# Kernel tuning notes

Measured on AMD Instinct MI355X. Metric: run time of the kernel, lower is better.

## Reference

```python
import jax, jax.numpy as jnp
import numpy as np

N, C, T, V, E = 4, 64, 64, 1024, 4096
IN_CH, OUT_CH, H = 256, 512, 8
DH = OUT_CH // H


def _leaky(x):
    return jnp.where(x >= 0, x, 0.01 * x)


def _mlp(x, w1, b1, w2, b2, g, b):
    # Linear -> LeakyReLU -> (dropout: eval identity) -> Linear -> BatchNorm(batch stats) -> LeakyReLU
    h = _leaky(x @ w1 + b1)
    h = h @ w2 + b2
    n, e, f = h.shape
    flat = h.reshape(n * e, f)
    mu = flat.mean(0)
    var = flat.var(0)  # biased variance, as torch BatchNorm uses for normalization
    flat = (flat - mu) * jax.lax.rsqrt(var + 1e-5) * g + b
    return _leaky(flat.reshape(n, e, f))


def _attn(q, k, v, wq, bq, wk, bk, wv, bv, wf, bf):
    # SelfAttention with scale=1: embed dim == OUT_CH, H heads of DH dims
    n, lq, _ = q.shape
    def split(t):
        return t.reshape(n, -1, H, DH).transpose(0, 2, 1, 3)  # (n, H, L, DH)
    Q = split(q @ wq + bq)
    K = split(k @ wk + bk)
    Vv = split(v @ wv + bv)
    scale = jnp.sqrt(jnp.float32(DH))
    att = jax.nn.softmax(jnp.einsum("nhqd,nhkd->nhqk", Q, K) / scale, axis=-1)
    x = jnp.einsum("nhqk,nhkd->nhqd", att, Vv)
    x = x.transpose(0, 2, 1, 3).reshape(n, lq, OUT_CH)
    return x @ wf + bf


def setup_inputs():
    key = jax.random.key(0)
    ks = list(jax.random.split(key, 24))

    def lin(k1, n_in, n_out):
        w = jax.random.normal(k1, (n_in, n_out), jnp.float32) * np.sqrt(2.0 / (n_in + n_out))
        b = jnp.full((n_out,), 0.1, jnp.float32)
        return w, b

    inp = {
        "x1": jax.random.normal(ks[0], (N, C, T, V), jnp.float32),
        "x2": jax.random.normal(ks[1], (N, C, T, V), jnp.float32),
        "encode1": jax.random.uniform(ks[2], (E, V), dtype=jnp.float32),
        "encode2": jax.random.uniform(ks[3], (E, V), dtype=jnp.float32),
    }
    i = 4
    for name in ("mlp", "nlp"):
        inp[name + "_w1"], inp[name + "_b1"] = lin(ks[i], 2 * IN_CH, OUT_CH); i += 1
        inp[name + "_w2"], inp[name + "_b2"] = lin(ks[i], OUT_CH, OUT_CH); i += 1
        inp[name + "_gamma"] = jnp.ones((OUT_CH,), jnp.float32)
        inp[name + "_beta"] = jnp.zeros((OUT_CH,), jnp.float32)
    for name in ("att1", "att2"):
        for p in ("wq", "wk", "wv", "fc"):
            inp[name + "_" + p + "_w"], inp[name + "_" + p + "_b"] = lin(ks[i], OUT_CH, OUT_CH); i += 1
    return inp


def reference(x1, x2, encode1, encode2,
              mlp_w1, mlp_b1, mlp_w2, mlp_b2, mlp_gamma, mlp_beta,
              nlp_w1, nlp_b1, nlp_w2, nlp_b2, nlp_gamma, nlp_beta,
              att1_wq_w, att1_wq_b, att1_wk_w, att1_wk_b, att1_wv_w, att1_wv_b, att1_fc_w, att1_fc_b,
              att2_wq_w, att2_wq_b, att2_wk_w, att2_wk_b, att2_wv_w, att2_wv_b, att2_fc_w, att2_fc_b):
    n, c, t, v = x1.shape

    def prep(x):
        # permute(0,2,3,1).view(N,V,-1) then AdaptiveAvgPool1d(IN_CH) with exact windows
        x = jnp.transpose(x, (0, 2, 3, 1)).reshape(n, v, t * c)
        return x.reshape(n, v, IN_CH, (t * c) // IN_CH).mean(-1)

    x1p = prep(x1)
    x2p = prep(x2)

    def node_enc(x):
        return jnp.concatenate([
            jnp.einsum("ev,nvc->nec", encode1, x),
            jnp.einsum("ev,nvc->nec", encode2, x),
        ], axis=-1)  # (N, E, 2*IN_CH)

    h1 = _mlp(node_enc(x1p), mlp_w1, mlp_b1, mlp_w2, mlp_b2, mlp_gamma, mlp_beta)
    h2 = _mlp(node_enc(x2p), nlp_w1, nlp_b1, nlp_w2, nlp_b2, nlp_gamma, nlp_beta)

    def edge_enc(h):
        r = jnp.einsum("ev,nec->nvc", encode1, h)  # (N, V, OUT_CH)
        return r / r.shape[1]

    e1 = edge_enc(h1)
    e2 = edge_enc(h2)

    a1 = _attn(e2, e1, e1, att1_wq_w, att1_wq_b, att1_wk_w, att1_wk_b, att1_wv_w, att1_wv_b, att1_fc_w, att1_fc_b)
    a2 = _attn(e1, e2, e2, att2_wq_w, att2_wq_b, att2_wk_w, att2_wk_b, att2_wv_w, att2_wv_b, att2_fc_w, att2_fc_b)

    c1 = jnp.concatenate([a1, a2], axis=1)  # (N, 2V, OUT_CH)
    c2 = jnp.concatenate([a2, a1], axis=1)
    A = jax.nn.softmax(jnp.einsum("nic,njc->nij", c1, c2), axis=-1)  # (N, 2V, 2V)
    # normalize_dynamic_digraph: AGCN-style column-degree normalization A @ D^{-1}
    col = A.sum(axis=1, keepdims=True)
    return A * jnp.where(col > 0, 1.0 / col, 0.0)
```

## Files before the change

kernel.cpp:

```cpp
#include <hip/hip_runtime.h>
#include <hip/hip_bf16.h>

#define LEAKY(v) ((v) >= 0.f ? (v) : 0.01f * (v))

typedef __attribute__((ext_vector_type(8))) short short8b;
typedef __attribute__((ext_vector_type(4))) float f32x4;
typedef __attribute__((ext_vector_type(4))) unsigned short us4;

__device__ __forceinline__ unsigned short f2b(float f) {
  unsigned int u = __builtin_bit_cast(unsigned int, f);
  return (unsigned short)((u + 0x7FFFu + ((u >> 16) & 1u)) >> 16);
}
__device__ __forceinline__ float b2f(unsigned short s) {
  return __builtin_bit_cast(float, (unsigned int)s << 16);
}

__device__ __forceinline__ void gload16(const unsigned short* g, unsigned short* l) {
  __builtin_amdgcn_global_load_lds(
      (const __attribute__((address_space(1))) unsigned int*)(g),
      (__attribute__((address_space(3))) unsigned int*)(l), 16, 0, 0);
}

__device__ __forceinline__ void stage64(const unsigned short* g, int ldg,
                                        unsigned short* lds, int lane, int w) {
  const int r8 = lane >> 3;
  const int ce = ((lane & 7) ^ r8) << 3;
  const int r0 = w * 8 + r8;
  gload16(g + (long)r0 * ldg + ce, lds + w * 512);
  gload16(g + (long)(r0 + 32) * ldg + ce, lds + 2048 + w * 512);
}

__device__ __forceinline__ short8b ldsw(const unsigned short* base, int row, int c4) {
  return *(const short8b*)&base[row * 64 + (((c4 ^ (row & 7)) << 3))];
}

struct WPtrs { const float* p[12]; float sc[12]; };

__global__ __launch_bounds__(256) void prologue_misc(
    const float* __restrict__ X1, const float* __restrict__ X2,
    float* __restrict__ S, const float* __restrict__ enc1,
    const float* __restrict__ enc2, unsigned short* __restrict__ ENC,
    unsigned short* __restrict__ E1T, WPtrs wp,
    unsigned short* __restrict__ WT) {
  __shared__ float t[64][65];
  const int b = blockIdx.x;
  const int tid = threadIdx.x;
  if (b < 2048) {
#pragma unroll
    for (int it = 0; it < 4; ++it) {
      const int lb = b + it * 2048;
      const int tt = lb & 63, y = (lb >> 6) & 15, z = lb >> 10;
      const float* X = (z >> 2) ? X2 : X1;
      const int n = z & 3;
      const long base = (((long)n * 64 + y * 4) * 64 + tt) * 1024 + tid * 4;
      const float4 a = *(const float4*)&X[base];
      const float4 bb = *(const float4*)&X[base + 65536];
      const float4 c = *(const float4*)&X[base + 2 * 65536];
      const float4 d = *(const float4*)&X[base + 3 * 65536];
      float4 o;
      o.x = (a.x + bb.x) + (c.x + d.x);
      o.y = (a.y + bb.y) + (c.y + d.y);
      o.z = (a.z + bb.z) + (c.z + d.z);
      o.w = (a.w + bb.w) + (c.w + d.w);
      *(float4*)&S[(((long)z * 16 + y) * 64 + tt) * 1024 + tid * 4] = o;
    }
  } else if (b < 4096) {
#pragma unroll
    for (int it = 0; it < 4; ++it) {
      const int cb = (b - 2048) + it * 2048;
      const int z = cb >> 12;
      const float* in = z ? enc2 : enc1;
      unsigned short* o = ENC + (long)z * (4L << 20);
      const long i = (long)(cb & 4095) * 256 + tid;
      const float4 v = ((const float4*)in)[i];
      us4 q;
      q[0] = f2b(v.x); q[1] = f2b(v.y); q[2] = f2b(v.z); q[3] = f2b(v.w);
      ((us4*)o)[i] = q;
    }
  } else if (b < 5120) {
    const int b3 = b - 4096;
    const int c0 = (b3 & 15) * 64, r0 = (b3 >> 4) * 64;
#pragma unroll
    for (int it = 0; it < 4; ++it) {
      int idx = tid + it * 256;
      int r = idx >> 4, c4 = (idx & 15) * 4;
      float4 v = *(const float4*)&enc1[(long)(r0 + r) * 1024 + c0 + c4];
      t[c4 + 0][r] = v.x; t[c4 + 1][r] = v.y;
      t[c4 + 2][r] = v.z; t[c4 + 3][r] = v.w;
    }
    __syncthreads();
#pragma unroll
    for (int it = 0; it < 4; ++it) {
      int idx = tid + it * 256;
      int c = idx >> 4, r4 = (idx & 15) * 4;
      us4 o;
      o[0] = f2b(t[c][r4 + 0]); o[1] = f2b(t[c][r4 + 1]);
      o[2] = f2b(t[c][r4 + 2]); o[3] = f2b(t[c][r4 + 3]);
      *(us4*)&E1T[(long)(c0 + c) * 4096 + r0 + r4] = o;
    }
  } else {
    const int b4 = b - 5120;
    const int x = b4 & 7, y = (b4 >> 3) & 7, z = b4 >> 6;
    const float* in = wp.p[z];
    const float s = wp.sc[z];
    unsigned short* ob = WT + (long)z * 262144;
    const int c0 = x * 64, r0 = y * 64;
#pragma unroll
    for (int it = 0; it < 4; ++it) {
      int idx = tid + it * 256;
      int r = idx >> 4, c4 = (idx & 15) * 4;
      float4 v = *(const float4*)&in[(long)(r0 + r) * 512 + c0 + c4];
      t[c4 + 0][r] = v.x; t[c4 + 1][r] = v.y;
      t[c4 + 2][r] = v.z; t[c4 + 3][r] = v.w;
    }
    __syncthreads();
#pragma unroll
    for (int it = 0; it < 4; ++it) {
      int idx = tid + it * 256;
      int c = idx >> 4, r4 = (idx & 15) * 4;
      us4 o;
      o[0] = f2b(t[c][r4 + 0] * s); o[1] = f2b(t[c][r4 + 1] * s);
      o[2] = f2b(t[c][r4 + 2] * s); o[3] = f2b(t[c][r4 + 3] * s);
      *(us4*)&ob[(long)(c0 + c) * 512 + r0 + r4] = o;
    }
  }
}

__global__ __launch_bounds__(256) void prep_finish(const float* __restrict__ S,
                                                   unsigned short* __restrict__ Pt) {
  const int t = blockIdx.x;
  const int cbi = blockIdx.y;
  const int z = blockIdx.z;
  const int n = z & 3, inp = z >> 2;
  const int tid = threadIdx.x;
  __shared__ unsigned short sacc[64][20];
  const long sb = (((long)z * 16 + cbi * 4) * 64 + t) * 1024 + tid * 4;
  const float4 a = *(const float4*)&S[sb];
  const float4 b = *(const float4*)&S[sb + 65536];
  const float4 c = *(const float4*)&S[sb + 2 * 65536];
  const float4 d = *(const float4*)&S[sb + 3 * 65536];
  float acc[4];
  acc[0] = (a.x + b.x) + (c.x + d.x);
  acc[1] = (a.y + b.y) + (c.y + d.y);
  acc[2] = (a.z + b.z) + (c.z + d.z);
  acc[3] = (a.w + b.w) + (c.w + d.w);
  const int q = tid & 15, vb = tid >> 4;
#pragma unroll
  for (int j = 0; j < 4; ++j)
    sacc[q * 4 + j][vb] = f2b(acc[j] * (1.f / 16.f));
  __syncthreads();
  const int vvv = tid >> 2, iq = tid & 3;
  const us4 o = *(const us4*)&sacc[vvv][iq * 4];
  *(us4*)&Pt[(long)inp * (1L << 20) + (long)n * 262144 +
             (long)(vvv * 4 + cbi) * 1024 + t * 16 + iq * 4] = o;
}

__global__ __launch_bounds__(256) void addcvt4(const unsigned short* __restrict__ P,
                                               unsigned short* __restrict__ out) {
#pragma unroll
  for (int it = 0; it < 4; ++it) {
    const long i = ((long)(blockIdx.x + it * 1024) * 256 + threadIdx.x) * 4;
    const us4 a = *(const us4*)&P[i];
    const us4 b = *(const us4*)&P[i + 4194304];
    const us4 c = *(const us4*)&P[i + 2 * 4194304];
    const us4 d = *(const us4*)&P[i + 3 * 4194304];
    us4 o;
#pragma unroll
    for (int j = 0; j < 4; ++j)
      o[j] = f2b((b2f(a[j]) + b2f(b[j])) + (b2f(c[j]) + b2f(d[j])));
    *(us4*)&out[i] = o;
  }
}

struct GDesc { const unsigned short* A; const unsigned short* B; long coff;
               const float* bias; int mode; float bscale; };
struct GDescs { GDesc d[16]; };

template <int ACT, int CMODE, int KSPLIT>
__global__ __launch_bounds__(256) void gemm_z(
    GDescs ga, void* __restrict__ Cv, int K, int lda, int ldb, int ldc,
    long sC2, float alpha) {
  const int bz = blockIdx.z;
  const int s = (KSPLIT > 1) ? (bz % KSPLIT) : 0;
  const int zb = (KSPLIT > 1) ? (bz / KSPLIT) : bz;
  const GDesc g = ga.d[zb];
  const unsigned short* Ab = g.A + (long)s * K;
  const unsigned short* Bb = g.B + (long)s * K;
  const int m0 = blockIdx.y * 128, n0 = blockIdx.x * 128;
  const int tid = threadIdx.x;
  const int lane = tid & 63, w = tid >> 6;
  const int wr = (w >> 1) * 64, wc = (w & 1) * 64;
  __shared__ unsigned short As[128 * 64];
  __shared__ unsigned short Bs[128 * 64];
  f32x4 acc[4][4];
#pragma unroll
  for (int i = 0; i < 4; ++i)
#pragma unroll
    for (int j = 0; j < 4; ++j) acc[i][j] = (f32x4){0.f, 0.f, 0.f, 0.f};
  const int srow = tid >> 3;
  const int scol = (((tid & 7) ^ ((tid >> 3) & 7)) << 3);
  const int rl = lane & 15, lg = lane >> 4, rx = rl & 7;
  for (int k0 = 0; k0 < K; k0 += 64) {
    __syncthreads();
#pragma unroll
    for (int it = 0; it < 4; ++it) {
      gload16(Ab + (long)(m0 + it * 32 + srow) * lda + k0 + scol,
              As + w * 512 + it * 2048);
      gload16(Bb + (long)(n0 + it * 32 + srow) * ldb + k0 + scol,
              Bs + w * 512 + it * 2048);
    }
    __syncthreads();
#pragma unroll
    for (int kk = 0; kk < 2; ++kk) {
      short8b af[4], bfr[4];
#pragma unroll
      for (int m = 0; m < 4; ++m)
        af[m] = *(const short8b*)&As[(wr + m * 16 + rl) * 64 +
                                     ((((kk * 4 + lg) ^ rx)) << 3)];
#pragma unroll
      for (int nn = 0; nn < 4; ++nn)
        bfr[nn] = *(const short8b*)&Bs[(wc + nn * 16 + rl) * 64 +
                                       ((((kk * 4 + lg) ^ rx)) << 3)];
#pragma unroll
      for (int m = 0; m < 4; ++m)
#pragma unroll
        for (int nn = 0; nn < 4; ++nn)
          acc[m][nn] = __builtin_amdgcn_mfma_f32_16x16x32_bf16(
              af[m], bfr[nn], acc[m][nn], 0, 0, 0);
    }
  }
  const int rrow = lg * 4;
  float bv[4];
#pragma unroll
  for (int nn = 0; nn < 4; ++nn)
    bv[nn] = g.bias ? g.bias[n0 + wc + nn * 16 + rl] * g.bscale : 0.f;
  const bool vt_layout = (CMODE == 2) || (CMODE == 4 && g.mode == 2);
  if (CMODE == 2 || CMODE == 4) {
    if (vt_layout) {
#pragma unroll
      for (int m = 0; m < 4; ++m)
#pragma unroll
        for (int nn = 0; nn < 4; ++nn) {
          const int row = m0 + wr + m * 16 + rrow;
          const int col = n0 + wc + nn * 16 + rl;
          us4 o;
#pragma unroll
          for (int r = 0; r < 4; ++r) {
            float v = alpha * acc[m][nn][r] + bv[nn];
            if (ACT == 1) v = LEAKY(v);
            o[r] = f2b(v);
          }
          const long off = g.coff + (long)(row >> 10) * 524288 +
                           (long)col * 1024 + (row & 1023);
          *(us4*)&((unsigned short*)Cv)[off] = o;
        }
    } else {
#pragma unroll
      for (int m = 0; m < 4; ++m)
#pragma unroll
        for (int nn = 0; nn < 4; ++nn)
#pragma unroll
          for (int r = 0; r < 4; ++r) {
            float v = alpha * acc[m][nn][r] + bv[nn];
            if (ACT == 1) v = LEAKY(v);
            const long off = g.coff +
                             (long)(m0 + wr + m * 16 + rrow + r) * ldc + n0 +
                             wc + nn * 16 + rl;
            ((unsigned short*)Cv)[off] = f2b(v);
          }
    }
  } else if (CMODE == 3) {
#pragma unroll
    for (int m = 0; m < 4; ++m)
#pragma unroll
      for (int nn = 0; nn < 4; ++nn) {
        const int row = m0 + wr + m * 16 + rrow;
        const int col = n0 + wc + nn * 16 + rl;
        us4 o;
#pragma unroll
        for (int r = 0; r < 4; ++r) {
          float v = alpha * acc[m][nn][r] + bv[nn];
          if (ACT == 1) v = LEAKY(v);
          o[r] = f2b(v);
        }
        *(us4*)&((unsigned short*)Cv)[g.coff + (long)col * ldc + row] = o;
      }
  } else {
#pragma unroll
    for (int m = 0; m < 4; ++m)
#pragma unroll
      for (int nn = 0; nn < 4; ++nn)
#pragma unroll
        for (int r = 0; r < 4; ++r) {
          float v = alpha * acc[m][nn][r] + bv[nn];
          if (ACT == 1) v = LEAKY(v);
          long off = g.coff + (long)s * sC2 +
                     (long)(m0 + wr + m * 16 + rrow + r) * ldc + n0 + wc +
                     nn * 16 + rl;
          if (CMODE == 1)
            ((unsigned short*)Cv)[off] = f2b(v);
          else
            ((float*)Cv)[off] = v;
        }
  }
}

__global__ __launch_bounds__(256) void bn_fused(
    unsigned short* __restrict__ X,
    const float* __restrict__ g1, const float* __restrict__ be1,
    const float* __restrict__ g2, const float* __restrict__ be2) {
  const int f = blockIdx.x;
  const int z = blockIdx.z;
  unsigned short* p = X + (long)z * (8L << 20) + (long)f * 16384;
  const int tid = threadIdx.x;
  us4 v[16];
  float s = 0.f, q = 0.f;
#pragma unroll
  for (int k = 0; k < 16; ++k) {
    v[k] = *(const us4*)&p[(k * 256 + tid) * 4];
#pragma unroll
    for (int j = 0; j < 4; ++j) {
      const float x = b2f(v[k][j]);
      s += x; q += x * x;
    }
  }
#pragma unroll
  for (int mask = 1; mask < 64; mask <<= 1) {
    s += __shfl_xor(s, mask, 64);
    q += __shfl_xor(q, mask, 64);
  }
  __shared__ float rs[8];
  const int wv = tid >> 6;
  if ((tid & 63) == 0) { rs[wv] = s; rs[4 + wv] = q; }
  __syncthreads();
  s = rs[0] + rs[1] + rs[2] + rs[3];
  q = rs[4] + rs[5] + rs[6] + rs[7];
  const float mu = s * (1.f / 16384.f);
  const float var = q * (1.f / 16384.f) - mu * mu;
  const float gg = (z ? g2 : g1)[f];
  const float bb0 = (z ? be2 : be1)[f];
  const float rstd = rsqrtf(var + 1e-5f) * gg;
  const float bb = bb0 - mu * rstd;
#pragma unroll
  for (int k = 0; k < 16; ++k) {
    us4 o;
#pragma unroll
    for (int j = 0; j < 4; ++j) {
      const float y = b2f(v[k][j]) * rstd + bb;
      o[j] = f2b(LEAKY(y));
    }
    *(us4*)&p[(k * 256 + tid) * 4] = o;
  }
}

__global__ __launch_bounds__(256) void attn_mfma(
    const unsigned short* __restrict__ Q, const unsigned short* __restrict__ K,
    const unsigned short* __restrict__ Vt, unsigned short* __restrict__ O) {
  const int qb = blockIdx.x, h = blockIdx.y;
  const int n = blockIdx.z & 3, sel = blockIdx.z >> 2;
  Q += (long)sel * 4194304;
  K += (long)sel * 4194304;
  Vt += (long)sel * 2097152;
  O += (long)sel * 2097152;
  const int tid = threadIdx.x;
  const int lane = tid & 63, w = tid >> 6;
  const int rl = lane & 15, lg = lane >> 4;
  __shared__ unsigned short Qs[4096];
  __shared__ unsigned short Ks[4096];
  __shared__ unsigned short Vs[4096];
  __shared__ unsigned short Ps[4096];
  stage64(Q + ((long)n * 1024 + qb * 64) * 512 + h * 64, 512, Qs, lane, w);
  __syncthreads();
  const int q = w * 16 + rl;
  const short8b qr0 = ldsw(Qs, q, lg);
  const short8b qr1 = ldsw(Qs, q, 4 + lg);
  float l_r = 0.f;
  f32x4 po[4];
#pragma unroll
  for (int i = 0; i < 4; ++i) po[i] = (f32x4){0.f, 0.f, 0.f, 0.f};
  const unsigned short* Kg0 = K + ((long)n * 1024) * 512 + h * 64;
  const unsigned short* Vg0 = Vt + (long)n * 524288 + (long)(h * 64) * 1024;
  for (int kt = 0; kt < 16; ++kt) {
    __syncthreads();
    stage64(Kg0 + (long)(kt * 64) * 512, 512, Ks, lane, w);
    stage64(Vg0 + kt * 64, 1024, Vs, lane, w);
    __syncthreads();
    f32x4 sa[4];
#pragma unroll
    for (int i = 0; i < 4; ++i) sa[i] = (f32x4){0.f, 0.f, 0.f, 0.f};
#pragma unroll
    for (int kk = 0; kk < 2; ++kk) {
      const short8b qf = kk ? qr1 : qr0;
#pragma unroll
      for (int mt = 0; mt < 4; ++mt) {
        const short8b kf = ldsw(Ks, mt * 16 + rl, 4 * kk + lg);
        sa[mt] = __builtin_amdgcn_mfma_f32_16x16x32_bf16(kf, qf, sa[mt], 0, 0, 0);
      }
    }
    float ps = 0.f;
#pragma unroll
    for (int mt = 0; mt < 4; ++mt) {
      us4 o;
#pragma unroll
      for (int r = 0; r < 4; ++r) {
        const float p = exp2f(sa[mt][r]);
        ps += p;
        o[r] = f2b(p);
      }
      const int c16 = (4 * mt + lg) >> 1;
      *(us4*)&Ps[q * 64 + ((c16 ^ (q & 7)) << 3) + ((lg & 1) << 2)] = o;
    }
    ps += __shfl_xor(ps, 16, 64);
    ps += __shfl_xor(ps, 32, 64);
    l_r += ps;
#pragma unroll
    for (int kk = 0; kk < 2; ++kk) {
      const short8b pf = ldsw(Ps, q, 4 * kk + lg);
#pragma unroll
      for (int nt = 0; nt < 4; ++nt) {
        const short8b vf = ldsw(Vs, nt * 16 + rl, 4 * kk + lg);
        po[nt] = __builtin_amdgcn_mfma_f32_16x16x32_bf16(pf, vf, po[nt], 0, 0, 0);
      }
    }
  }
  float invr[4];
#pragma unroll
  for (int r = 0; r < 4; ++r) invr[r] = 1.f / __shfl(l_r, lg * 4 + r, 64);
  const long ob = ((long)n * 1024 + qb * 64 + w * 16) * 512 + h * 64;
#pragma unroll
  for (int nt = 0; nt < 4; ++nt)
#pragma unroll
    for (int r = 0; r < 4; ++r)
      O[ob + (long)(lg * 4 + r) * 512 + nt * 16 + rl] = f2b(po[nt][r] * invr[r]);
}

__global__ __launch_bounds__(256) void softmax_cs(const float* __restrict__ D,
                                                  float* __restrict__ RS,
                                                  float* __restrict__ CS) {
  __shared__ float colacc[2048];
  __shared__ float red[8];
  const int tid = threadIdx.x;
  const int wv = tid >> 6, ln = tid & 63;
#pragma unroll
  for (int k = 0; k < 8; ++k) colacc[tid + k * 256] = 0.f;
  __syncthreads();
  const int r0 = blockIdx.x * 8;
  const int n = r0 >> 11;
  for (int rr = 0; rr < 8; ++rr) {
    const float* p = D + (long)(r0 + rr) * 2048;
    float v[8];
    float mx = -1e30f;
#pragma unroll
    for (int k = 0; k < 8; ++k) {
      v[k] = p[tid + k * 256];
      mx = fmaxf(mx, v[k]);
    }
#pragma unroll
    for (int mask = 1; mask < 64; mask <<= 1) mx = fmaxf(mx, __shfl_xor(mx, mask, 64));
    if (ln == 0) red[wv] = mx;
    __syncthreads();
    mx = fmaxf(fmaxf(red[0], red[1]), fmaxf(red[2], red[3]));
    float sum = 0.f;
#pragma unroll
    for (int k = 0; k < 8; ++k) {
      v[k] = __expf(v[k] - mx);
      sum += v[k];
    }
#pragma unroll
    for (int mask = 1; mask < 64; mask <<= 1) sum += __shfl_xor(sum, mask, 64);
    if (ln == 0) red[4 + wv] = sum;
    __syncthreads();
    sum = red[4] + red[5] + red[6] + red[7];
    const float inv = 1.f / sum;
    if (tid == 0) {
      RS[(r0 + rr) * 2] = mx;
      RS[(r0 + rr) * 2 + 1] = inv;
    }
#pragma unroll
    for (int k = 0; k < 8; ++k) colacc[tid + k * 256] += v[k] * inv;
    __syncthreads();
  }
#pragma unroll
  for (int k = 0; k < 8; ++k)
    atomicAdd(&CS[n * 2048 + tid + k * 256], colacc[tid + k * 256]);
}

__global__ __launch_bounds__(256) void final_scale(float* __restrict__ D,
                                                   const float* __restrict__ RS,
                                                   const float* __restrict__ CS) {
#pragma unroll
  for (int it = 0; it < 8; ++it) {
    const long i = ((long)(blockIdx.x + it * 2048) * 256 + threadIdx.x) * 4;
    const long row = i >> 11;
    const int n = (int)(row >> 11);
    const int j = (int)(i & 2047);
    const float mx = RS[row * 2];
    const float inv = RS[row * 2 + 1];
    float4 v = *(float4*)&D[i];
    const float* c = &CS[n * 2048 + j];
    v.x = __expf(v.x - mx) * inv * (c[0] > 0.f ? 1.f / c[0] : 0.f);
    v.y = __expf(v.y - mx) * inv * (c[1] > 0.f ? 1.f / c[1] : 0.f);
    v.z = __expf(v.z - mx) * inv * (c[2] > 0.f ? 1.f / c[2] : 0.f);
    v.w = __expf(v.w - mx) * inv * (c[3] > 0.f ? 1.f / c[3] : 0.f);
    *(float4*)&D[i] = v;
  }
}

extern "C" void kernel_launch(void* const* d_in, const int* in_sizes, int n_in,
                              void* d_out, int out_size, void* d_ws,
                              size_t ws_size, hipStream_t stream) {
  const float* x1 = (const float*)d_in[0];
  const float* x2 = (const float*)d_in[1];
  const float* enc1 = (const float*)d_in[2];
  const float* enc2 = (const float*)d_in[3];
  const float* mlp_b1 = (const float*)d_in[5];
  const float* mlp_b2 = (const float*)d_in[7];
  const float* mlp_g = (const float*)d_in[8];
  const float* mlp_be = (const float*)d_in[9];
  const float* nlp_b1 = (const float*)d_in[11];
  const float* nlp_b2 = (const float*)d_in[13];
  const float* nlp_g = (const float*)d_in[14];
  const float* nlp_be = (const float*)d_in[15];
  float* out = (float*)d_out;

  unsigned short* W = (unsigned short*)d_ws;
  const long M1 = 1L << 20;
  const long S = 262144;
  const float K2 = 0.18033688f;
  unsigned short* Pt = W;
  unsigned short* ENC = W + 4 * M1;
  unsigned short* E1T = W + 12 * M1;
  unsigned short* WT = W + 16 * M1;
  unsigned short* NE = W + 20 * M1;
  unsigned short* H1T = W + 20 * M1;
  unsigned short* MID = W + 36 * M1;
  float* Sprep = (float*)(W + 36 * M1);
  unsigned short* PB = W + 36 * M1;
  unsigned short* E1 = W + 4 * M1;
  unsigned short* E2 = W + 6 * M1;
  unsigned short* QKV = W + 36 * M1;
  unsigned short* VT = W + 44 * M1;
  unsigned short* AO = W + 48 * M1;
  unsigned short* A1P = W + 8 * M1;
  unsigned short* A2P = W + 10 * M1;
  float* ST = (float*)(W + 56 * M1);
  float* CS = ST + 2048;
  float* RS = CS + 8192;

  const dim3 T(256);
  const long sP = 262144;
  const long sNE = 2097152;
  const long sE = 524288;
  const long sD = 4194304;

  hipMemsetAsync(CS, 0, 8192 * sizeof(float), stream);

  WPtrs wp;
  wp.p[0] = (const float*)d_in[4];   wp.sc[0] = 1.f;
  wp.p[1] = (const float*)d_in[6];   wp.sc[1] = 1.f;
  wp.p[2] = (const float*)d_in[10];  wp.sc[2] = 1.f;
  wp.p[3] = (const float*)d_in[12];  wp.sc[3] = 1.f;
  wp.p[4] = (const float*)d_in[16];  wp.sc[4] = K2;
  wp.p[5] = (const float*)d_in[18];  wp.sc[5] = 1.f;
  wp.p[6] = (const float*)d_in[24];  wp.sc[6] = K2;
  wp.p[7] = (const float*)d_in[26];  wp.sc[7] = 1.f;
  wp.p[8] = (const float*)d_in[20];  wp.sc[8] = 1.f;
  wp.p[9] = (const float*)d_in[28];  wp.sc[9] = 1.f;
  wp.p[10] = (const float*)d_in[22]; wp.sc[10] = 1.f;
  wp.p[11] = (const float*)d_in[30]; wp.sc[11] = 1.f;
  prologue_misc<<<5888, T, 0, stream>>>(x1, x2, Sprep, enc1, enc2, ENC, E1T,
                                        wp, WT);
  prep_finish<<<dim3(64, 4, 8), T, 0, stream>>>(Sprep, Pt);

  {
    GDescs g{};
    for (int inp = 0; inp < 2; ++inp)
      for (int pr = 0; pr < 2; ++pr)
        for (int nn = 0; nn < 4; ++nn)
          g.d[inp * 8 + pr * 4 + nn] = {
              ENC + (long)pr * (4 * M1), Pt + (long)inp * M1 + nn * sP,
              (long)inp * (8 * M1) + (long)nn * sNE + pr * 256, nullptr, 0, 1.f};
    gemm_z<0, 1, 1><<<dim3(2, 32, 16), T, 0, stream>>>(g, NE, 1024, 1024,
                                                       1024, 512, 0, 1.f);
  }
  {
    GDescs g{};
    g.d[0] = {NE, WT + 0 * S, 0, mlp_b1, 0, 1.f};
    g.d[1] = {NE + 8 * M1, WT + 2 * S, 8 * M1, nlp_b1, 0, 1.f};
    gemm_z<1, 1, 1><<<dim3(4, 128, 2), T, 0, stream>>>(g, MID, 512, 512, 512,
                                                       512, 0, 1.f);
  }
  {
    GDescs g{};
    g.d[0] = {MID, WT + 1 * S, 0, mlp_b2, 0, 1.f};
    g.d[1] = {MID + 8 * M1, WT + 3 * S, 8 * M1, nlp_b2, 0, 1.f};
    gemm_z<0, 3, 1><<<dim3(4, 128, 2), T, 0, stream>>>(g, H1T, 512, 512, 512,
                                                       16384, 0, 1.f);
  }
  bn_fused<<<dim3(512, 1, 2), T, 0, stream>>>(H1T, mlp_g, mlp_be, nlp_g, nlp_be);

  {
    GDescs g{};
    for (int d = 0; d < 8; ++d)
      g.d[d] = {E1T, H1T + (long)(d >> 2) * (8 * M1) + (d & 3) * 4096,
                (long)d * 524288, nullptr, 0, 1.f};
    gemm_z<0, 1, 4><<<dim3(4, 8, 32), T, 0, stream>>>(g, PB, 1024, 4096,
                                                      16384, 512, 4194304,
                                                      1.f / 1024.f);
  }
  addcvt4<<<1024, T, 0, stream>>>(PB, E1);

  {
    GDescs g{};
    g.d[0] = {E2, WT + 4 * S, 0, (const float*)d_in[17], 1, K2};
    g.d[1] = {E1, WT + 5 * S, 2 * M1, (const float*)d_in[19], 1, 1.f};
    g.d[2] = {E1, WT + 6 * S, 4 * M1, (const float*)d_in[25], 1, K2};
    g.d[3] = {E2, WT + 7 * S, 6 * M1, (const float*)d_in[27], 1, 1.f};
    g.d[4] = {E1, WT + 8 * S, 8 * M1, (const float*)d_in[21], 2, 1.f};
    g.d[5] = {E2, WT + 9 * S, 10 * M1, (const float*)d_in[29], 2, 1.f};
    gemm_z<0, 4, 1><<<dim3(4, 32, 6), T, 0, stream>>>(g, QKV, 512, 512, 512,
                                                      512, 0, 1.f);
  }

  attn_mfma<<<dim3(16, 8, 8), T, 0, stream>>>(QKV, QKV + 2 * M1, VT, AO);

  {
    GDescs g{};
    g.d[0] = {AO, WT + 10 * S, 0, (const float*)d_in[23], 0, 1.f};
    g.d[1] = {AO + 2 * M1, WT + 11 * S, 2 * M1, (const float*)d_in[31], 0, 1.f};
    gemm_z<0, 1, 1><<<dim3(4, 32, 2), T, 0, stream>>>(g, A1P, 512, 512, 512,
                                                      512, 0, 1.f);
  }

  {
    GDescs g{};
    for (int q = 0; q < 4; ++q)
      for (int n = 0; n < 4; ++n) {
        const unsigned short* A = (q < 2 ? A1P : A2P) + n * sE;
        const unsigned short* B = ((q == 0 || q == 2) ? A2P : A1P) + n * sE;
        const long coff =
            (long)n * sD + (q & 1) * 1024 + (long)(q >> 1) * 2097152;
        g.d[q * 4 + n] = {A, B, coff, nullptr, 0, 1.f};
      }
    gemm_z<0, 0, 1><<<dim3(8, 8, 16), T, 0, stream>>>(g, out, 512, 512, 512,
                                                      2048, 0, 1.f);
  }

  softmax_cs<<<1024, T, 0, stream>>>(out, RS, CS);
  final_scale<<<2048, T, 0, stream>>>(out, RS, CS);
}
```

Before: 382.9 us.

## Pool input in one pass and split the fused prologue into separate kernels

The channel pooling of x1/x2 used to be two stages: a partial sum written to a float scratch buffer, then read back by a finish kernel. Each block now loads all 16 channel slices directly and reduces them in registers, so the intermediate scratch write and re-read disappear. The fused multi-role prologue kernel is also split into separate kernels for pooling, encoder bf16 conversion, encoder transpose and weight transpose, with occupancy hints on some of them. The cost is more kernel launches and higher register pressure in the pooling kernel, which holds 16 float4 loads per thread.

```diff
diff --git a/kernel.cpp b/kernel.cpp
--- a/kernel.cpp
+++ b/kernel.cpp
@@ -34,125 +34,111 @@
   return *(const short8b*)&base[row * 64 + (((c4 ^ (row & 7)) << 3))];
 }
 
-struct WPtrs { const float* p[12]; float sc[12]; };
-
-__global__ __launch_bounds__(256) void prologue_misc(
+__global__ __launch_bounds__(256, 4) void prep_pool_t(
     const float* __restrict__ X1, const float* __restrict__ X2,
-    float* __restrict__ S, const float* __restrict__ enc1,
-    const float* __restrict__ enc2, unsigned short* __restrict__ ENC,
-    unsigned short* __restrict__ E1T, WPtrs wp,
-    unsigned short* __restrict__ WT) {
-  __shared__ float t[64][65];
-  const int b = blockIdx.x;
-  const int tid = threadIdx.x;
-  if (b < 2048) {
-#pragma unroll
-    for (int it = 0; it < 4; ++it) {
-      const int lb = b + it * 2048;
-      const int tt = lb & 63, y = (lb >> 6) & 15, z = lb >> 10;
-      const float* X = (z >> 2) ? X2 : X1;
-      const int n = z & 3;
-      const long base = (((long)n * 64 + y * 4) * 64 + tt) * 1024 + tid * 4;
-      const float4 a = *(const float4*)&X[base];
-      const float4 bb = *(const float4*)&X[base + 65536];
-      const float4 c = *(const float4*)&X[base + 2 * 65536];
-      const float4 d = *(const float4*)&X[base + 3 * 65536];
-      float4 o;
-      o.x = (a.x + bb.x) + (c.x + d.x);
-      o.y = (a.y + bb.y) + (c.y + d.y);
-      o.z = (a.z + bb.z) + (c.z + d.z);
-      o.w = (a.w + bb.w) + (c.w + d.w);
-      *(float4*)&S[(((long)z * 16 + y) * 64 + tt) * 1024 + tid * 4] = o;
-    }
-  } else if (b < 4096) {
-#pragma unroll
-    for (int it = 0; it < 4; ++it) {
-      const int cb = (b - 2048) + it * 2048;
-      const int z = cb >> 12;
-      const float* in = z ? enc2 : enc1;
-      unsigned short* o = ENC + (long)z * (4L << 20);
-      const long i = (long)(cb & 4095) * 256 + tid;
-      const float4 v = ((const float4*)in)[i];
-      us4 q;
-      q[0] = f2b(v.x); q[1] = f2b(v.y); q[2] = f2b(v.z); q[3] = f2b(v.w);
-      ((us4*)o)[i] = q;
-    }
-  } else if (b < 5120) {
-    const int b3 = b - 4096;
-    const int c0 = (b3 & 15) * 64, r0 = (b3 >> 4) * 64;
-#pragma unroll
-    for (int it = 0; it < 4; ++it) {
-      int idx = tid + it * 256;
-      int r = idx >> 4, c4 = (idx & 15) * 4;
-      float4 v = *(const float4*)&enc1[(long)(r0 + r) * 1024 + c0 + c4];
-      t[c4 + 0][r] = v.x; t[c4 + 1][r] = v.y;
-      t[c4 + 2][r] = v.z; t[c4 + 3][r] = v.w;
-    }
-    __syncthreads();
-#pragma unroll
-    for (int it = 0; it < 4; ++it) {
-      int idx = tid + it * 256;
-      int c = idx >> 4, r4 = (idx & 15) * 4;
-      us4 o;
-      o[0] = f2b(t[c][r4 + 0]); o[1] = f2b(t[c][r4 + 1]);
-      o[2] = f2b(t[c][r4 + 2]); o[3] = f2b(t[c][r4 + 3]);
-      *(us4*)&E1T[(long)(c0 + c) * 4096 + r0 + r4] = o;
-    }
-  } else {
-    const int b4 = b - 5120;
-    const int x = b4 & 7, y = (b4 >> 3) & 7, z = b4 >> 6;
-    const float* in = wp.p[z];
-    const float s = wp.sc[z];
-    unsigned short* ob = WT + (long)z * 262144;
-    const int c0 = x * 64, r0 = y * 64;
-#pragma unroll
-    for (int it = 0; it < 4; ++it) {
-      int idx = tid + it * 256;
-      int r = idx >> 4, c4 = (idx & 15) * 4;
-      float4 v = *(const float4*)&in[(long)(r0 + r) * 512 + c0 + c4];
-      t[c4 + 0][r] = v.x; t[c4 + 1][r] = v.y;
-      t[c4 + 2][r] = v.z; t[c4 + 3][r] = v.w;
-    }
-    __syncthreads();
-#pragma unroll
-    for (int it = 0; it < 4; ++it) {
-      int idx = tid + it * 256;
-      int c = idx >> 4, r4 = (idx & 15) * 4;
-      us4 o;
-      o[0] = f2b(t[c][r4 + 0] * s); o[1] = f2b(t[c][r4 + 1] * s);
-      o[2] = f2b(t[c][r4 + 2] * s); o[3] = f2b(t[c][r4 + 3] * s);
-      *(us4*)&ob[(long)(c0 + c) * 512 + r0 + r4] = o;
-    }
-  }
-}
-
-__global__ __launch_bounds__(256) void prep_finish(const float* __restrict__ S,
-                                                   unsigned short* __restrict__ Pt) {
+    unsigned short* __restrict__ Pt) {
   const int t = blockIdx.x;
   const int cbi = blockIdx.y;
-  const int z = blockIdx.z;
-  const int n = z & 3, inp = z >> 2;
+  const int n = blockIdx.z & 3, inp = blockIdx.z >> 2;
+  const float* X = inp ? X2 : X1;
   const int tid = threadIdx.x;
   __shared__ unsigned short sacc[64][20];
-  const long sb = (((long)z * 16 + cbi * 4) * 64 + t) * 1024 + tid * 4;
-  const float4 a = *(const float4*)&S[sb];
-  const float4 b = *(const float4*)&S[sb + 65536];
-  const float4 c = *(const float4*)&S[sb + 2 * 65536];
-  const float4 d = *(const float4*)&S[sb + 3 * 65536];
-  float acc[4];
-  acc[0] = (a.x + b.x) + (c.x + d.x);
-  acc[1] = (a.y + b.y) + (c.y + d.y);
-  acc[2] = (a.z + b.z) + (c.z + d.z);
-  acc[3] = (a.w + b.w) + (c.w + d.w);
+  const long base0 = (((long)n * 64 + cbi * 16) * 64 + t) * 1024 + tid * 4;
+  f32x4 v[16];
+#pragma unroll
+  for (int m = 0; m < 16; ++m)
+    v[m] = *(const f32x4*)&X[base0 + (long)m * 65536];
   const int q = tid & 15, vb = tid >> 4;
 #pragma unroll
-  for (int j = 0; j < 4; ++j)
-    sacc[q * 4 + j][vb] = f2b(acc[j] * (1.f / 16.f));
+  for (int j = 0; j < 4; ++j) {
+    float s = ((v[0][j] + v[1][j]) + (v[2][j] + v[3][j])) +
+              ((v[4][j] + v[5][j]) + (v[6][j] + v[7][j]));
+    s += ((v[8][j] + v[9][j]) + (v[10][j] + v[11][j])) +
+         ((v[12][j] + v[13][j]) + (v[14][j] + v[15][j]));
+    sacc[q * 4 + j][vb] = f2b(s * (1.f / 16.f));
+  }
   __syncthreads();
   const int vvv = tid >> 2, iq = tid & 3;
   const us4 o = *(const us4*)&sacc[vvv][iq * 4];
   *(us4*)&Pt[(long)inp * (1L << 20) + (long)n * 262144 +
              (long)(vvv * 4 + cbi) * 1024 + t * 16 + iq * 4] = o;
+}
+
+__global__ __launch_bounds__(256, 4) void convert2_f2b(
+    const float* __restrict__ i1, const float* __restrict__ i2,
+    unsigned short* __restrict__ out) {
+  const int tid = threadIdx.x;
+  f32x4 v[4];
+  long oidx[4];
+#pragma unroll
+  for (int it = 0; it < 4; ++it) {
+    const int cb = blockIdx.x + it * 2048;
+    const int z = cb >> 12;
+    const float* in = z ? i2 : i1;
+    const long i = (long)(cb & 4095) * 256 + tid;
+    v[it] = ((const f32x4*)in)[i];
+    oidx[it] = (long)z * (1L << 20) + i;
+  }
+#pragma unroll
+  for (int it = 0; it < 4; ++it) {
+    us4 q;
+    q[0] = f2b(v[it][0]); q[1] = f2b(v[it][1]);
+    q[2] = f2b(v[it][2]); q[3] = f2b(v[it][3]);
+    ((us4*)out)[oidx[it]] = q;
+  }
+}
+
+__global__ __launch_bounds__(256) void transpose_f2b(
+    const float* __restrict__ in, unsigned short* __restrict__ out, int R, int C) {
+  __shared__ float t[64][65];
+  const int c0 = blockIdx.x * 64, r0 = blockIdx.y * 64;
+  const int tid = threadIdx.x;
+#pragma unroll
+  for (int it = 0; it < 4; ++it) {
+    int idx = tid + it * 256;
+    int r = idx >> 4, c4 = (idx & 15) * 4;
+    float4 v = *(const float4*)&in[(long)(r0 + r) * C + c0 + c4];
+    t[c4 + 0][r] = v.x; t[c4 + 1][r] = v.y;
+    t[c4 + 2][r] = v.z; t[c4 + 3][r] = v.w;
+  }
+  __syncthreads();
+#pragma unroll
+  for (int it = 0; it < 4; ++it) {
+    int idx = tid + it * 256;
+    int c = idx >> 4, r4 = (idx & 15) * 4;
+    us4 o;
+    o[0] = f2b(t[c][r4 + 0]); o[1] = f2b(t[c][r4 + 1]);
+    o[2] = f2b(t[c][r4 + 2]); o[3] = f2b(t[c][r4 + 3]);
+    *(us4*)&out[(long)(c0 + c) * R + r0 + r4] = o;
+  }
+}
+
+struct WPtrs { const float* p[12]; float sc[12]; };
+__global__ __launch_bounds__(256) void wtrans(WPtrs wp, unsigned short* __restrict__ out) {
+  const float* in = wp.p[blockIdx.z];
+  const float s = wp.sc[blockIdx.z];
+  unsigned short* ob = out + (long)blockIdx.z * 262144;
+  __shared__ float t[64][65];
+  const int c0 = blockIdx.x * 64, r0 = blockIdx.y * 64;
+  const int tid = threadIdx.x;
+#pragma unroll
+  for (int it = 0; it < 4; ++it) {
+    int idx = tid + it * 256;
+    int r = idx >> 4, c4 = (idx & 15) * 4;
+    float4 v = *(const float4*)&in[(long)(r0 + r) * 512 + c0 + c4];
+    t[c4 + 0][r] = v.x; t[c4 + 1][r] = v.y;
+    t[c4 + 2][r] = v.z; t[c4 + 3][r] = v.w;
+  }
+  __syncthreads();
+#pragma unroll
+  for (int it = 0; it < 4; ++it) {
+    int idx = tid + it * 256;
+    int c = idx >> 4, r4 = (idx & 15) * 4;
+    us4 o;
+    o[0] = f2b(t[c][r4 + 0] * s); o[1] = f2b(t[c][r4 + 1] * s);
+    o[2] = f2b(t[c][r4 + 2] * s); o[3] = f2b(t[c][r4 + 3] * s);
+    *(us4*)&ob[(long)(c0 + c) * 512 + r0 + r4] = o;
+  }
 }
 
 __global__ __launch_bounds__(256) void addcvt4(const unsigned short* __restrict__ P,
@@ -534,7 +520,6 @@
   unsigned short* NE = W + 20 * M1;
   unsigned short* H1T = W + 20 * M1;
   unsigned short* MID = W + 36 * M1;
-  float* Sprep = (float*)(W + 36 * M1);
   unsigned short* PB = W + 36 * M1;
   unsigned short* E1 = W + 4 * M1;
   unsigned short* E2 = W + 6 * M1;
@@ -555,6 +540,9 @@
 
   hipMemsetAsync(CS, 0, 8192 * sizeof(float), stream);
 
+  prep_pool_t<<<dim3(64, 4, 8), T, 0, stream>>>(x1, x2, Pt);
+  convert2_f2b<<<2048, T, 0, stream>>>(enc1, enc2, ENC);
+  transpose_f2b<<<dim3(16, 64), T, 0, stream>>>(enc1, E1T, 4096, 1024);
   WPtrs wp;
   wp.p[0] = (const float*)d_in[4];   wp.sc[0] = 1.f;
   wp.p[1] = (const float*)d_in[6];   wp.sc[1] = 1.f;
@@ -568,9 +556,7 @@
   wp.p[9] = (const float*)d_in[28];  wp.sc[9] = 1.f;
   wp.p[10] = (const float*)d_in[22]; wp.sc[10] = 1.f;
   wp.p[11] = (const float*)d_in[30]; wp.sc[11] = 1.f;
-  prologue_misc<<<5888, T, 0, stream>>>(x1, x2, Sprep, enc1, enc2, ENC, E1T,
-                                        wp, WT);
-  prep_finish<<<dim3(64, 4, 8), T, 0, stream>>>(Sprep, Pt);
+  wtrans<<<dim3(8, 8, 12), T, 0, stream>>>(wp, WT);
 
   {
     GDescs g{};
```

Measured after the change: 379.0 us. No clear change (-1.0%).
